# Kernel optimization log

Hardware: AMD Instinct MI355X
Metric: run time of the kernel (lower is better)

## Reference

```python
import jax, jax.numpy as jnp
import numpy as np

HIDDEN = 1024
HEADS = 16
HEAD_DIM = HIDDEN // HEADS
GAMMA = 0.5
B, S = 2, 2048


def setup_inputs() -> dict:
    key = jax.random.key(0)
    ks = jax.random.split(key, 9)
    sc = 1.0 / np.sqrt(HIDDEN)
    x = jax.random.normal(ks[0], (B, S, HIDDEN), dtype=jnp.float32)
    attn_mask = jnp.zeros((S, S), dtype=bool)  # True = masked; all-False here
    Wq = jax.random.normal(ks[1], (HIDDEN, HIDDEN), dtype=jnp.float32) * sc
    bq = jnp.zeros((HIDDEN,), dtype=jnp.float32)
    Wk = jax.random.normal(ks[2], (HIDDEN, HIDDEN), dtype=jnp.float32) * sc
    bk = jnp.zeros((HIDDEN,), dtype=jnp.float32)
    Wv = jax.random.normal(ks[3], (HIDDEN, HIDDEN), dtype=jnp.float32) * sc
    bv = jnp.zeros((HIDDEN,), dtype=jnp.float32)
    Wo = jax.random.normal(ks[4], (HIDDEN, HIDDEN), dtype=jnp.float32) * sc
    bo = jnp.zeros((HIDDEN,), dtype=jnp.float32)
    return {"x": x, "attn_mask": attn_mask, "Wq": Wq, "bq": bq,
            "Wk": Wk, "bk": bk, "Wv": Wv, "bv": bv, "Wo": Wo, "bo": bo}


def reference(x, attn_mask, Wq, bq, Wk, bk, Wv, bv, Wo, bo):
    Bn, Sn, _ = x.shape
    # projections (torch Linear: x @ W.T + b), reshape to [B, H, S, Dh]
    def proj(W, b):
        y = x @ W.T + b
        return y.reshape(Bn, Sn, HEADS, HEAD_DIM).transpose(0, 2, 1, 3)
    q, k, v = proj(Wq, bq), proj(Wk, bk), proj(Wv, bv)
    scores = jnp.einsum('bhqd,bhkd->bhqk', q, k) / np.sqrt(HEAD_DIM)
    # diversity bias: cosine similarity of raw x (F.normalize eps=1e-12)
    normed = x / jnp.maximum(jnp.linalg.norm(x, axis=-1, keepdims=True), 1e-12)
    sim = jnp.einsum('bqd,bkd->bqk', normed, normed)
    scores = scores - GAMMA * sim[:, None, :, :]
    scores = jnp.where(attn_mask[None, None, :, :], -jnp.inf, scores)
    probs = jax.nn.softmax(scores, axis=-1)
    ctx = jnp.einsum('bhqk,bhkd->bhqd', probs, v)
    ctx = ctx.transpose(0, 2, 1, 3).reshape(Bn, Sn, HIDDEN)
    return ctx @ Wo.T + bo
```

## Files before the change

### kernel.cpp

```cpp
#include <hip/hip_runtime.h>

#define HID 1024
#define SEQ 2048
#define NB 2
#define NH 16
#define HD 64

#define C1 0.1803368801111204f
#define C2 0.7213475204444817f

typedef __attribute__((ext_vector_type(8))) short bf16x8;
typedef __attribute__((ext_vector_type(8))) unsigned short u16x8;
typedef __attribute__((ext_vector_type(4))) float f32x4;

__device__ __forceinline__ unsigned short f2bf(float f) {
  unsigned u = __builtin_bit_cast(unsigned, f);
  u += 0x7fffu + ((u >> 16) & 1u);
  return (unsigned short)(u >> 16);
}
__device__ __forceinline__ float bf2f(unsigned short u) {
  return __builtin_bit_cast(float, ((unsigned)u) << 16);
}

#define GLOAD16(gsrc, ldst)                                                     \
  __builtin_amdgcn_global_load_lds(                                             \
      (const __attribute__((address_space(1))) void*)(gsrc),                    \
      (__attribute__((address_space(3))) void*)(ldst), 16, 0, 0)

__global__ __launch_bounds__(256) void convert_w_kernel(
    const float* __restrict__ Wq, const float* __restrict__ Wk,
    const float* __restrict__ Wv, const float* __restrict__ Wo,
    unsigned short* __restrict__ Wb) {
  int i = blockIdx.x * 256 + threadIdx.x;
  const int per = (HID * HID) / 8;
  int m = i / per;
  const float* sp = (m == 0) ? Wq : (m == 1) ? Wk : (m == 2) ? Wv : Wo;
  int j = (i - m * per) * 8;
  const float4* p = reinterpret_cast<const float4*>(sp + j);
  float4 a = p[0], b = p[1];
  u16x8 o;
  o[0] = f2bf(a.x); o[1] = f2bf(a.y); o[2] = f2bf(a.z); o[3] = f2bf(a.w);
  o[4] = f2bf(b.x); o[5] = f2bf(b.y); o[6] = f2bf(b.z); o[7] = f2bf(b.w);
  *reinterpret_cast<u16x8*>(Wb + (size_t)i * 8) = o;
}

__global__ __launch_bounds__(256) void rownorm_kernel(
    const float* __restrict__ x, unsigned short* __restrict__ xb,
    unsigned short* __restrict__ nxb) {
  int row = blockIdx.x, tid = threadIdx.x;
  const float4 v = reinterpret_cast<const float4*>(x + (size_t)row * HID)[tid];
  float ss = v.x * v.x + v.y * v.y + v.z * v.z + v.w * v.w;
#pragma unroll
  for (int off = 32; off; off >>= 1) ss += __shfl_xor(ss, off, 64);
  __shared__ float wsum[4];
  if ((tid & 63) == 0) wsum[tid >> 6] = ss;
  __syncthreads();
  float tot = wsum[0] + wsum[1] + wsum[2] + wsum[3];
  float inv = 1.0f / fmaxf(sqrtf(tot), 1e-12f);
  ushort4 a, b;
  a.x = f2bf(v.x); a.y = f2bf(v.y); a.z = f2bf(v.z); a.w = f2bf(v.w);
  b.x = f2bf(v.x * inv); b.y = f2bf(v.y * inv);
  b.z = f2bf(v.z * inv); b.w = f2bf(v.w * inv);
  reinterpret_cast<ushort4*>(xb  + (size_t)row * HID)[tid] = a;
  reinterpret_cast<ushort4*>(nxb + (size_t)row * HID)[tid] = b;
}

template <int MODE>
__global__ __launch_bounds__(256) void gemm_nt(
    const unsigned short* __restrict__ A, long strideA,
    const unsigned short* __restrict__ B, long strideB,
    void* __restrict__ Cv, long strideC, int ldc,
    int M, int N, int K,
    const float* __restrict__ b0, const float* __restrict__ b1,
    const float* __restrict__ b2, const unsigned char* __restrict__ mask) {
  __shared__ __align__(16) unsigned short As[128][40];
  __shared__ __align__(16) unsigned short Bs[128][40];
  int tid = threadIdx.x, lane = tid & 63, wid = tid >> 6;
  int g = lane >> 4, lr = lane & 15;
  int wr = wid >> 1, wc = wid & 1;
  int m0 = blockIdx.y * 128, n0 = blockIdx.x * 128;
  const unsigned short* Ab = A + (size_t)blockIdx.z * strideA;
  const unsigned short* Bb = B + (size_t)blockIdx.z * strideB;
  f32x4 acc[4][4] = {};
  for (int k0 = 0; k0 < K; k0 += 32) {
#pragma unroll
    for (int p = 0; p < 2; p++) {
      int u = tid + p * 256;
      int row = u >> 2, chk = u & 3;
      *reinterpret_cast<u16x8*>(&As[row][chk * 8]) =
          *reinterpret_cast<const u16x8*>(Ab + (size_t)(m0 + row) * K + k0 + chk * 8);
      *reinterpret_cast<u16x8*>(&Bs[row][chk * 8]) =
          *reinterpret_cast<const u16x8*>(Bb + (size_t)(n0 + row) * K + k0 + chk * 8);
    }
    __syncthreads();
    bf16x8 af[4], bfr[4];
#pragma unroll
    for (int i = 0; i < 4; i++) {
      af[i]  = *reinterpret_cast<const bf16x8*>(&As[wr * 64 + i * 16 + lr][g * 8]);
      bfr[i] = *reinterpret_cast<const bf16x8*>(&Bs[wc * 64 + i * 16 + lr][g * 8]);
    }
#pragma unroll
    for (int i = 0; i < 4; i++)
#pragma unroll
      for (int j = 0; j < 4; j++)
        acc[i][j] = __builtin_amdgcn_mfma_f32_16x16x32_bf16(af[i], bfr[j], acc[i][j], 0, 0, 0);
    __syncthreads();
  }
#pragma unroll
  for (int i = 0; i < 4; i++)
#pragma unroll
    for (int j = 0; j < 4; j++) {
      int col = n0 + wc * 64 + j * 16 + lr;
#pragma unroll
      for (int r = 0; r < 4; r++) {
        int row = m0 + wr * 64 + i * 16 + 4 * g + r;
        float v = acc[i][j][r];
        if (MODE == 0) {
          const float* bp = (col < 1024) ? b0 : (col < 2048 ? b1 : b2);
          v += bp[col & 1023];
          ((unsigned short*)Cv)[(size_t)blockIdx.z * strideC + (size_t)row * ldc + col] = f2bf(v);
        } else if (MODE == 1) {
          float t = -C2 * v + (mask[(size_t)row * N + col] ? -1e30f : 0.0f);
          ((unsigned short*)Cv)[(size_t)blockIdx.z * strideC + (size_t)row * ldc + col] = f2bf(t);
        } else {
          v += b0[col];
          ((float*)Cv)[(size_t)blockIdx.z * strideC + (size_t)row * ldc + col] = v;
        }
      }
    }
}

__global__ __launch_bounds__(512) void flash_kernel(
    const unsigned short* __restrict__ QKV,
    const unsigned short* __restrict__ D2,
    unsigned short* __restrict__ ctxb) {
  int qt = blockIdx.x, h = blockIdx.y, b = blockIdx.z;
  int tid = threadIdx.x, wid = tid >> 6, lane = tid & 63;
  int g = lane >> 4, lr = lane & 15;
  __shared__ __align__(16) unsigned short Ks[2][64 * 64];
  __shared__ __align__(16) unsigned short Vt[2][64 * 64];
  __shared__ __align__(16) unsigned short Pl[8][16 * 72];
  const size_t ld = 3 * HID;
  const size_t bS = (size_t)b * SEQ;

  const unsigned short* qp = QKV + (bS + qt * 128 + wid * 16 + lr) * ld + h * HD;
  bf16x8 qf0 = *reinterpret_cast<const bf16x8*>(qp + g * 8);
  bf16x8 qf1 = *reinterpret_cast<const bf16x8*>(qp + 32 + g * 8);

  const unsigned short* gK = QKV + (bS + wid * 8 + (lane >> 3)) * ld + HID + h * HD
                             + (((lane & 7) ^ (lane >> 3)) << 3);
  const unsigned short* gV = QKV + (bS + (tid >> 3)) * ld + 2 * HID + h * HD + ((tid & 7) << 3);
  const int ch = tid & 7, kr3 = (tid >> 3) & 7, kb = tid >> 6;
  const int vtbase = ch * 512 + kr3;
  const int pre7 = (kb ^ ch) & 7;

  const unsigned short* bD = D2 + (size_t)b * SEQ * SEQ
                             + (size_t)(qt * 128 + wid * 16 + lr) * SEQ + 4 * g;

  GLOAD16(gK, &Ks[0][0] + wid * 512);
  {
    u16x8 vv = *reinterpret_cast<const u16x8*>(gV);
#pragma unroll
    for (int i = 0; i < 8; i++)
      Vt[0][vtbase + i * 64 + ((pre7 ^ i) << 3)] = vv[i];
  }
  __syncthreads();

  f32x4 acc[4] = {};
  float mrun = -1e30f, lrun = 0.0f;
  const int kb0 = lr * 64 + ((g ^ (lr & 7)) << 3);

  for (int kt = 0; kt < 32; ++kt) {
    const int cb = kt & 1;
    const unsigned short* ks = &Ks[cb][0];
    const unsigned short* vt = &Vt[cb][0];
    u16x8 vv2 = {};
    if (kt < 31) {
      GLOAD16(gK + (size_t)(kt + 1) * 64 * ld, &Ks[cb ^ 1][0] + wid * 512);
      vv2 = *reinterpret_cast<const u16x8*>(gV + (size_t)(kt + 1) * 64 * ld);
    }
    ushort4 bv4[4];
#pragma unroll
    for (int kc = 0; kc < 4; kc++)
      bv4[kc] = *reinterpret_cast<const ushort4*>(bD + kt * 64 + kc * 16);

    f32x4 s[4];
#pragma unroll
    for (int kc = 0; kc < 4; kc++) {
      bf16x8 kf0 = *reinterpret_cast<const bf16x8*>(ks + kc * 1024 + kb0);
      bf16x8 kf1 = *reinterpret_cast<const bf16x8*>(ks + kc * 1024 + (kb0 ^ 32));
      f32x4 z = {};
      z = __builtin_amdgcn_mfma_f32_16x16x32_bf16(kf0, qf0, z, 0, 0, 0);
      s[kc] = __builtin_amdgcn_mfma_f32_16x16x32_bf16(kf1, qf1, z, 0, 0, 0);
    }
    float mx = mrun;
#pragma unroll
    for (int kc = 0; kc < 4; kc++) {
      s[kc][0] = fmaf(s[kc][0], C1, bf2f(bv4[kc].x));
      s[kc][1] = fmaf(s[kc][1], C1, bf2f(bv4[kc].y));
      s[kc][2] = fmaf(s[kc][2], C1, bf2f(bv4[kc].z));
      s[kc][3] = fmaf(s[kc][3], C1, bf2f(bv4[kc].w));
      mx = fmaxf(mx, fmaxf(fmaxf(s[kc][0], s[kc][1]), fmaxf(s[kc][2], s[kc][3])));
    }
    mx = fmaxf(mx, __shfl_xor(mx, 16, 64));
    mx = fmaxf(mx, __shfl_xor(mx, 32, 64));
    float sc = exp2f(mrun - mx);
    mrun = mx;
    float rs = 0.0f;
#pragma unroll
    for (int kc = 0; kc < 4; kc++) {
      float p0 = exp2f(s[kc][0] - mx), p1 = exp2f(s[kc][1] - mx);
      float p2 = exp2f(s[kc][2] - mx), p3 = exp2f(s[kc][3] - mx);
      rs += (p0 + p1) + (p2 + p3);
      ushort4 pk;
      pk.x = f2bf(p0); pk.y = f2bf(p1); pk.z = f2bf(p2); pk.w = f2bf(p3);
      *reinterpret_cast<ushort4*>(&Pl[wid][lr * 72 + kc * 16 + 4 * g]) = pk;
    }
    rs += __shfl_xor(rs, 16, 64);
    rs += __shfl_xor(rs, 32, 64);
    lrun = lrun * sc + rs;
    float s0 = __shfl(sc, 4 * g + 0, 16), s1 = __shfl(sc, 4 * g + 1, 16);
    float s2 = __shfl(sc, 4 * g + 2, 16), s3 = __shfl(sc, 4 * g + 3, 16);
#pragma unroll
    for (int df = 0; df < 4; df++) {
      acc[df][0] *= s0; acc[df][1] *= s1; acc[df][2] *= s2; acc[df][3] *= s3;
    }
    if (kt < 31) {
#pragma unroll
      for (int i = 0; i < 8; i++)
        Vt[cb ^ 1][vtbase + i * 64 + ((pre7 ^ i) << 3)] = vv2[i];
    }
#pragma unroll
    for (int c2 = 0; c2 < 2; c2++) {
      bf16x8 pf = *reinterpret_cast<const bf16x8*>(&Pl[wid][lr * 72 + c2 * 32 + g * 8]);
#pragma unroll
      for (int df = 0; df < 4; df++) {
        int blk = ((4 * c2 + g) ^ (lr & 7) ^ ((df * 2 + (lr >> 3)) & 7)) & 7;
        bf16x8 vf = *reinterpret_cast<const bf16x8*>(vt + (df * 16 + lr) * 64 + (blk << 3));
        acc[df] = __builtin_amdgcn_mfma_f32_16x16x32_bf16(pf, vf, acc[df], 0, 0, 0);
      }
    }
    __syncthreads();
  }
  float l0 = 1.0f / __shfl(lrun, 4 * g + 0, 16);
  float l1 = 1.0f / __shfl(lrun, 4 * g + 1, 16);
  float l2 = 1.0f / __shfl(lrun, 4 * g + 2, 16);
  float l3 = 1.0f / __shfl(lrun, 4 * g + 3, 16);
  unsigned short* op = ctxb + (bS + qt * 128 + wid * 16 + 4 * g) * HID + h * HD + lr;
#pragma unroll
  for (int df = 0; df < 4; df++) {
    op[0 * HID + df * 16] = f2bf(acc[df][0] * l0);
    op[1 * HID + df * 16] = f2bf(acc[df][1] * l1);
    op[2 * HID + df * 16] = f2bf(acc[df][2] * l2);
    op[3 * HID + df * 16] = f2bf(acc[df][3] * l3);
  }
}

extern "C" void kernel_launch(void* const* d_in, const int* in_sizes, int n_in,
                              void* d_out, int out_size, void* d_ws, size_t ws_size,
                              hipStream_t stream) {
  const float* x = (const float*)d_in[0];
  const unsigned char* mask = (const unsigned char*)d_in[1];
  const float* Wq = (const float*)d_in[2];
  const float* bq = (const float*)d_in[3];
  const float* Wk = (const float*)d_in[4];
  const float* bk = (const float*)d_in[5];
  const float* Wv = (const float*)d_in[6];
  const float* bv = (const float*)d_in[7];
  const float* Wo = (const float*)d_in[8];
  const float* bo = (const float*)d_in[9];
  float* out = (float*)d_out;

  char* ws = (char*)d_ws;
  const size_t MiB = 1024 * 1024;
  unsigned short* xb  = (unsigned short*)(ws + 0 * MiB);
  unsigned short* nxb = (unsigned short*)(ws + 8 * MiB);
  unsigned short* Wb  = (unsigned short*)(ws + 16 * MiB);
  unsigned short* QKV = (unsigned short*)(ws + 24 * MiB);
  unsigned short* D2  = (unsigned short*)(ws + 48 * MiB);
  unsigned short* ctx = (unsigned short*)(ws + 64 * MiB);

  convert_w_kernel<<<2048, 256, 0, stream>>>(Wq, Wk, Wv, Wo, Wb);
  rownorm_kernel<<<NB * SEQ, 256, 0, stream>>>(x, xb, nxb);
  gemm_nt<0><<<dim3(24, 32, 1), 256, 0, stream>>>(
      xb, 0, Wb, 0, QKV, 0, 3 * HID, NB * SEQ, 3 * HID, HID, bq, bk, bv, nullptr);
  gemm_nt<1><<<dim3(16, 16, 2), 256, 0, stream>>>(
      nxb, (long)SEQ * HID, nxb, (long)SEQ * HID, D2, (long)SEQ * SEQ, SEQ,
      SEQ, SEQ, HID, nullptr, nullptr, nullptr, mask);
  flash_kernel<<<dim3(SEQ / 128, NH, NB), 512, 0, stream>>>(QKV, D2, ctx);
  gemm_nt<2><<<dim3(8, 32, 1), 256, 0, stream>>>(
      ctx, 0, Wb + (size_t)3 * HID * HID, 0, out, 0, HID, NB * SEQ, HID, HID,
      bo, nullptr, nullptr, nullptr);
}
```

Measured before the change: 231.4 us.

## Give each flash-attention wave two query tiles and skip redundant rescaling

The flash kernel now runs 4 waves of 256 threads per block instead of 8, with each wave owning 32 query rows split into two 16-row halves. Each K/V fragment read from LDS is reused across both halves. The online-softmax rescale runs only when some row max grows by more than 8 in log2 units. Row sums are accumulated with an MFMA against a vector of ones instead of shuffle reductions, and probabilities are packed to bf16 by truncation via a byte permute. These changes cut LDS traffic, cross-lane shuffles and VALU work, at the cost of higher register pressure, fewer waves per block, and slightly different rounding of P.

Result: faster. 220.6 us (-4.6%).

```diff
diff --git a/kernel.cpp b/kernel.cpp
--- a/kernel.cpp
+++ b/kernel.cpp
@@ -130,7 +130,7 @@
     }
 }
 
-__global__ __launch_bounds__(512) void flash_kernel(
+__global__ __launch_bounds__(256, 3) void flash_kernel(
     const unsigned short* __restrict__ QKV,
     const unsigned short* __restrict__ D2,
     unsigned short* __restrict__ ctxb) {
@@ -139,120 +139,175 @@
   int g = lane >> 4, lr = lane & 15;
   __shared__ __align__(16) unsigned short Ks[2][64 * 64];
   __shared__ __align__(16) unsigned short Vt[2][64 * 64];
-  __shared__ __align__(16) unsigned short Pl[8][16 * 72];
+  __shared__ __align__(16) unsigned short Pl[4][32 * 72];
   const size_t ld = 3 * HID;
   const size_t bS = (size_t)b * SEQ;
-
-  const unsigned short* qp = QKV + (bS + qt * 128 + wid * 16 + lr) * ld + h * HD;
-  bf16x8 qf0 = *reinterpret_cast<const bf16x8*>(qp + g * 8);
-  bf16x8 qf1 = *reinterpret_cast<const bf16x8*>(qp + 32 + g * 8);
-
-  const unsigned short* gK = QKV + (bS + wid * 8 + (lane >> 3)) * ld + HID + h * HD
-                             + (((lane & 7) ^ (lane >> 3)) << 3);
-  const unsigned short* gV = QKV + (bS + (tid >> 3)) * ld + 2 * HID + h * HD + ((tid & 7) << 3);
-  const int ch = tid & 7, kr3 = (tid >> 3) & 7, kb = tid >> 6;
+  const int qbase = qt * 128 + wid * 32;
+
+  const unsigned short* qp = QKV + (bS + qbase + lr) * ld + h * HD + g * 8;
+  bf16x8 qf00 = *reinterpret_cast<const bf16x8*>(qp);
+  bf16x8 qf01 = *reinterpret_cast<const bf16x8*>(qp + 32);
+  bf16x8 qf10 = *reinterpret_cast<const bf16x8*>(qp + 16 * ld);
+  bf16x8 qf11 = *reinterpret_cast<const bf16x8*>(qp + 16 * ld + 32);
+
+  const unsigned short* gK0 = QKV + (bS + wid * 16 + (lane >> 3)) * ld + HID + h * HD
+                              + (((lane & 7) ^ (lane >> 3)) << 3);
+  const unsigned short* gK1 = gK0 + 8 * ld;
+
+  const int vr0 = tid >> 3, ch = tid & 7;
+  const unsigned short* gV0 = QKV + (bS + vr0) * ld + 2 * HID + h * HD + (ch << 3);
+  const unsigned short* gV1 = gV0 + 32 * ld;
+  const int kr3 = vr0 & 7;
+  const int kb0v = vr0 >> 3, kb1v = kb0v + 4;
   const int vtbase = ch * 512 + kr3;
-  const int pre7 = (kb ^ ch) & 7;
-
-  const unsigned short* bD = D2 + (size_t)b * SEQ * SEQ
-                             + (size_t)(qt * 128 + wid * 16 + lr) * SEQ + 4 * g;
-
-  GLOAD16(gK, &Ks[0][0] + wid * 512);
+  const int pre0 = (kb0v ^ ch) & 7, pre1 = (kb1v ^ ch) & 7;
+
+  const unsigned short* bD0 = D2 + (size_t)b * SEQ * SEQ
+                              + (size_t)(qbase + lr) * SEQ + 4 * g;
+  const unsigned short* bD1 = bD0 + (size_t)16 * SEQ;
+
+  GLOAD16(gK0, &Ks[0][wid * 1024]);
+  GLOAD16(gK1, &Ks[0][wid * 1024 + 512]);
   {
-    u16x8 vv = *reinterpret_cast<const u16x8*>(gV);
-#pragma unroll
-    for (int i = 0; i < 8; i++)
-      Vt[0][vtbase + i * 64 + ((pre7 ^ i) << 3)] = vv[i];
+    u16x8 v0 = *reinterpret_cast<const u16x8*>(gV0);
+    u16x8 v1 = *reinterpret_cast<const u16x8*>(gV1);
+#pragma unroll
+    for (int i = 0; i < 8; i++) {
+      Vt[0][vtbase + i * 64 + ((pre0 ^ i) << 3)] = v0[i];
+      Vt[0][vtbase + i * 64 + ((pre1 ^ i) << 3)] = v1[i];
+    }
   }
   __syncthreads();
 
-  f32x4 acc[4] = {};
-  float mrun = -1e30f, lrun = 0.0f;
+  f32x4 acc[2][4] = {};
+  f32x4 rsacc[2] = {};
+  float mrun[2] = {-1e30f, -1e30f};
   const int kb0 = lr * 64 + ((g ^ (lr & 7)) << 3);
+  bf16x8 ones;
+#pragma unroll
+  for (int i = 0; i < 8; i++) ones[i] = 0x3F80;
 
   for (int kt = 0; kt < 32; ++kt) {
     const int cb = kt & 1;
     const unsigned short* ks = &Ks[cb][0];
     const unsigned short* vt = &Vt[cb][0];
-    u16x8 vv2 = {};
+    u16x8 vv0 = {}, vv1 = {};
     if (kt < 31) {
-      GLOAD16(gK + (size_t)(kt + 1) * 64 * ld, &Ks[cb ^ 1][0] + wid * 512);
-      vv2 = *reinterpret_cast<const u16x8*>(gV + (size_t)(kt + 1) * 64 * ld);
-    }
-    ushort4 bv4[4];
-#pragma unroll
-    for (int kc = 0; kc < 4; kc++)
-      bv4[kc] = *reinterpret_cast<const ushort4*>(bD + kt * 64 + kc * 16);
-
-    f32x4 s[4];
+      GLOAD16(gK0 + (size_t)(kt + 1) * 64 * ld, &Ks[cb ^ 1][wid * 1024]);
+      GLOAD16(gK1 + (size_t)(kt + 1) * 64 * ld, &Ks[cb ^ 1][wid * 1024 + 512]);
+      vv0 = *reinterpret_cast<const u16x8*>(gV0 + (size_t)(kt + 1) * 64 * ld);
+      vv1 = *reinterpret_cast<const u16x8*>(gV1 + (size_t)(kt + 1) * 64 * ld);
+    }
+    ushort4 bv[2][4];
+#pragma unroll
+    for (int kc = 0; kc < 4; kc++) {
+      bv[0][kc] = *reinterpret_cast<const ushort4*>(bD0 + kt * 64 + kc * 16);
+      bv[1][kc] = *reinterpret_cast<const ushort4*>(bD1 + kt * 64 + kc * 16);
+    }
+    f32x4 s[2][4];
 #pragma unroll
     for (int kc = 0; kc < 4; kc++) {
       bf16x8 kf0 = *reinterpret_cast<const bf16x8*>(ks + kc * 1024 + kb0);
       bf16x8 kf1 = *reinterpret_cast<const bf16x8*>(ks + kc * 1024 + (kb0 ^ 32));
-      f32x4 z = {};
-      z = __builtin_amdgcn_mfma_f32_16x16x32_bf16(kf0, qf0, z, 0, 0, 0);
-      s[kc] = __builtin_amdgcn_mfma_f32_16x16x32_bf16(kf1, qf1, z, 0, 0, 0);
-    }
-    float mx = mrun;
-#pragma unroll
-    for (int kc = 0; kc < 4; kc++) {
-      s[kc][0] = fmaf(s[kc][0], C1, bf2f(bv4[kc].x));
-      s[kc][1] = fmaf(s[kc][1], C1, bf2f(bv4[kc].y));
-      s[kc][2] = fmaf(s[kc][2], C1, bf2f(bv4[kc].z));
-      s[kc][3] = fmaf(s[kc][3], C1, bf2f(bv4[kc].w));
-      mx = fmaxf(mx, fmaxf(fmaxf(s[kc][0], s[kc][1]), fmaxf(s[kc][2], s[kc][3])));
-    }
-    mx = fmaxf(mx, __shfl_xor(mx, 16, 64));
-    mx = fmaxf(mx, __shfl_xor(mx, 32, 64));
-    float sc = exp2f(mrun - mx);
-    mrun = mx;
-    float rs = 0.0f;
-#pragma unroll
-    for (int kc = 0; kc < 4; kc++) {
-      float p0 = exp2f(s[kc][0] - mx), p1 = exp2f(s[kc][1] - mx);
-      float p2 = exp2f(s[kc][2] - mx), p3 = exp2f(s[kc][3] - mx);
-      rs += (p0 + p1) + (p2 + p3);
-      ushort4 pk;
-      pk.x = f2bf(p0); pk.y = f2bf(p1); pk.z = f2bf(p2); pk.w = f2bf(p3);
-      *reinterpret_cast<ushort4*>(&Pl[wid][lr * 72 + kc * 16 + 4 * g]) = pk;
-    }
-    rs += __shfl_xor(rs, 16, 64);
-    rs += __shfl_xor(rs, 32, 64);
-    lrun = lrun * sc + rs;
-    float s0 = __shfl(sc, 4 * g + 0, 16), s1 = __shfl(sc, 4 * g + 1, 16);
-    float s2 = __shfl(sc, 4 * g + 2, 16), s3 = __shfl(sc, 4 * g + 3, 16);
-#pragma unroll
-    for (int df = 0; df < 4; df++) {
-      acc[df][0] *= s0; acc[df][1] *= s1; acc[df][2] *= s2; acc[df][3] *= s3;
+      f32x4 z0 = {};
+      z0 = __builtin_amdgcn_mfma_f32_16x16x32_bf16(kf0, qf00, z0, 0, 0, 0);
+      s[0][kc] = __builtin_amdgcn_mfma_f32_16x16x32_bf16(kf1, qf01, z0, 0, 0, 0);
+      f32x4 z1 = {};
+      z1 = __builtin_amdgcn_mfma_f32_16x16x32_bf16(kf0, qf10, z1, 0, 0, 0);
+      s[1][kc] = __builtin_amdgcn_mfma_f32_16x16x32_bf16(kf1, qf11, z1, 0, 0, 0);
+    }
+    float mx[2];
+#pragma unroll
+    for (int qh = 0; qh < 2; qh++) {
+      float m01, m23;
+#pragma unroll
+      for (int kc = 0; kc < 4; kc++) {
+        s[qh][kc][0] = fmaf(s[qh][kc][0], C1, bf2f(bv[qh][kc].x));
+        s[qh][kc][1] = fmaf(s[qh][kc][1], C1, bf2f(bv[qh][kc].y));
+        s[qh][kc][2] = fmaf(s[qh][kc][2], C1, bf2f(bv[qh][kc].z));
+        s[qh][kc][3] = fmaf(s[qh][kc][3], C1, bf2f(bv[qh][kc].w));
+      }
+      m01 = fmaxf(fmaxf(s[qh][0][0], s[qh][0][1]), fmaxf(s[qh][0][2], s[qh][0][3]));
+      m23 = fmaxf(fmaxf(s[qh][1][0], s[qh][1][1]), fmaxf(s[qh][1][2], s[qh][1][3]));
+      m01 = fmaxf(m01, fmaxf(fmaxf(s[qh][2][0], s[qh][2][1]), fmaxf(s[qh][2][2], s[qh][2][3])));
+      m23 = fmaxf(m23, fmaxf(fmaxf(s[qh][3][0], s[qh][3][1]), fmaxf(s[qh][3][2], s[qh][3][3])));
+      mx[qh] = fmaxf(m01, m23);
+    }
+    if (!__all((mx[0] <= mrun[0] + 8.0f) & (mx[1] <= mrun[1] + 8.0f))) {
+#pragma unroll
+      for (int qh = 0; qh < 2; qh++) {
+        float M = mx[qh];
+        M = fmaxf(M, __shfl_xor(M, 16, 64));
+        M = fmaxf(M, __shfl_xor(M, 32, 64));
+        M = fmaxf(M, mrun[qh]);
+        float sc = exp2f(mrun[qh] - M);
+        mrun[qh] = M;
+        float s0 = __shfl(sc, 4 * g + 0, 16), s1 = __shfl(sc, 4 * g + 1, 16);
+        float s2 = __shfl(sc, 4 * g + 2, 16), s3 = __shfl(sc, 4 * g + 3, 16);
+#pragma unroll
+        for (int df = 0; df < 4; df++) {
+          acc[qh][df][0] *= s0; acc[qh][df][1] *= s1;
+          acc[qh][df][2] *= s2; acc[qh][df][3] *= s3;
+        }
+        rsacc[qh][0] *= s0; rsacc[qh][1] *= s1;
+        rsacc[qh][2] *= s2; rsacc[qh][3] *= s3;
+      }
+    }
+#pragma unroll
+    for (int qh = 0; qh < 2; qh++) {
+#pragma unroll
+      for (int kc = 0; kc < 4; kc++) {
+        float p0 = exp2f(s[qh][kc][0] - mrun[qh]);
+        float p1 = exp2f(s[qh][kc][1] - mrun[qh]);
+        float p2 = exp2f(s[qh][kc][2] - mrun[qh]);
+        float p3 = exp2f(s[qh][kc][3] - mrun[qh]);
+        uint2 w;
+        w.x = __builtin_amdgcn_perm(__builtin_bit_cast(unsigned, p1),
+                                    __builtin_bit_cast(unsigned, p0), 0x07060302u);
+        w.y = __builtin_amdgcn_perm(__builtin_bit_cast(unsigned, p3),
+                                    __builtin_bit_cast(unsigned, p2), 0x07060302u);
+        *reinterpret_cast<uint2*>(&Pl[wid][(qh * 16 + lr) * 72 + kc * 16 + 4 * g]) = w;
+      }
     }
     if (kt < 31) {
 #pragma unroll
-      for (int i = 0; i < 8; i++)
-        Vt[cb ^ 1][vtbase + i * 64 + ((pre7 ^ i) << 3)] = vv2[i];
+      for (int i = 0; i < 8; i++) {
+        Vt[cb ^ 1][vtbase + i * 64 + ((pre0 ^ i) << 3)] = vv0[i];
+        Vt[cb ^ 1][vtbase + i * 64 + ((pre1 ^ i) << 3)] = vv1[i];
+      }
     }
 #pragma unroll
     for (int c2 = 0; c2 < 2; c2++) {
-      bf16x8 pf = *reinterpret_cast<const bf16x8*>(&Pl[wid][lr * 72 + c2 * 32 + g * 8]);
+      bf16x8 vf[4];
 #pragma unroll
       for (int df = 0; df < 4; df++) {
         int blk = ((4 * c2 + g) ^ (lr & 7) ^ ((df * 2 + (lr >> 3)) & 7)) & 7;
-        bf16x8 vf = *reinterpret_cast<const bf16x8*>(vt + (df * 16 + lr) * 64 + (blk << 3));
-        acc[df] = __builtin_amdgcn_mfma_f32_16x16x32_bf16(pf, vf, acc[df], 0, 0, 0);
+        vf[df] = *reinterpret_cast<const bf16x8*>(vt + (df * 16 + lr) * 64 + (blk << 3));
+      }
+#pragma unroll
+      for (int qh = 0; qh < 2; qh++) {
+        bf16x8 pf = *reinterpret_cast<const bf16x8*>(
+            &Pl[wid][(qh * 16 + lr) * 72 + c2 * 32 + g * 8]);
+        rsacc[qh] = __builtin_amdgcn_mfma_f32_16x16x32_bf16(pf, ones, rsacc[qh], 0, 0, 0);
+#pragma unroll
+        for (int df = 0; df < 4; df++)
+          acc[qh][df] = __builtin_amdgcn_mfma_f32_16x16x32_bf16(pf, vf[df], acc[qh][df], 0, 0, 0);
       }
     }
     __syncthreads();
   }
-  float l0 = 1.0f / __shfl(lrun, 4 * g + 0, 16);
-  float l1 = 1.0f / __shfl(lrun, 4 * g + 1, 16);
-  float l2 = 1.0f / __shfl(lrun, 4 * g + 2, 16);
-  float l3 = 1.0f / __shfl(lrun, 4 * g + 3, 16);
-  unsigned short* op = ctxb + (bS + qt * 128 + wid * 16 + 4 * g) * HID + h * HD + lr;
-#pragma unroll
-  for (int df = 0; df < 4; df++) {
-    op[0 * HID + df * 16] = f2bf(acc[df][0] * l0);
-    op[1 * HID + df * 16] = f2bf(acc[df][1] * l1);
-    op[2 * HID + df * 16] = f2bf(acc[df][2] * l2);
-    op[3 * HID + df * 16] = f2bf(acc[df][3] * l3);
+#pragma unroll
+  for (int qh = 0; qh < 2; qh++) {
+    float l0 = 1.0f / rsacc[qh][0], l1 = 1.0f / rsacc[qh][1];
+    float l2 = 1.0f / rsacc[qh][2], l3 = 1.0f / rsacc[qh][3];
+    unsigned short* op = ctxb + (bS + qbase + qh * 16 + 4 * g) * HID + h * HD + lr;
+#pragma unroll
+    for (int df = 0; df < 4; df++) {
+      op[0 * HID + df * 16] = f2bf(acc[qh][df][0] * l0);
+      op[1 * HID + df * 16] = f2bf(acc[qh][df][1] * l1);
+      op[2 * HID + df * 16] = f2bf(acc[qh][df][2] * l2);
+      op[3 * HID + df * 16] = f2bf(acc[qh][df][3] * l3);
+    }
   }
 }
 
@@ -287,7 +342,7 @@
   gemm_nt<1><<<dim3(16, 16, 2), 256, 0, stream>>>(
       nxb, (long)SEQ * HID, nxb, (long)SEQ * HID, D2, (long)SEQ * SEQ, SEQ,
       SEQ, SEQ, HID, nullptr, nullptr, nullptr, mask);
-  flash_kernel<<<dim3(SEQ / 128, NH, NB), 512, 0, stream>>>(QKV, D2, ctx);
+  flash_kernel<<<dim3(SEQ / 128, NH, NB), 256, 0, stream>>>(QKV, D2, ctx);
   gemm_nt<2><<<dim3(8, 32, 1), 256, 0, stream>>>(
       ctx, 0, Wb + (size_t)3 * HID * HID, 0, out, 0, HID, NB * SEQ, HID, HID,
       bo, nullptr, nullptr, nullptr);
```
